# Kernel optimization log

Measured on AMD Instinct MI355X. Metric: run time of the kernel, lower is better.

## Reference

```python
import jax, jax.numpy as jnp
import numpy as np


def setup_inputs() -> dict:
    key = jax.random.key(0)
    k1, k2 = jax.random.split(key)
    B, S, D = 4, 2048, 1024
    x = jax.random.normal(k1, (B, S, D), dtype=jnp.float32)
    # uniform initializer in keras is small; scale to keep softmax well-behaved
    kernel = jax.random.normal(k2, (3, D, D), dtype=jnp.float32) * 0.02
    return {"x": x, "kernel": kernel}


def reference(x, kernel):
    # x: [B, S, D], kernel: [3, D, D]
    D = x.shape[-1]
    q = jnp.einsum('bsd,de->bse', x, kernel[0])
    k = jnp.einsum('bsd,de->bse', x, kernel[1])
    v = jnp.einsum('bsd,de->bse', x, kernel[2])
    scores = jnp.einsum('bqe,bke->bqk', q, k) / jnp.sqrt(jnp.float32(D))
    attn = jax.nn.softmax(scores, axis=-1)
    return jnp.einsum('bqk,bke->bqe', attn, v)
```

## Files before the change

kernel.cpp:

```cpp
#include <hip/hip_runtime.h>
#include <hip/hip_bf16.h>
#include <cstdint>

typedef __bf16 bf16x8 __attribute__((ext_vector_type(8)));
typedef float f32x4 __attribute__((ext_vector_type(4)));

__device__ __forceinline__ unsigned short f2bf(float f) {
  union { float f; uint32_t u; } a; a.f = f;
  uint32_t r = a.u + 0x7fffu + ((a.u >> 16) & 1u);
  return (unsigned short)(r >> 16);
}
__device__ __forceinline__ void gload_lds16(const unsigned short* g, unsigned short* l) {
  __builtin_amdgcn_global_load_lds(
      (const __attribute__((address_space(1))) void*)g,
      (__attribute__((address_space(3))) void*)l, 16, 0, 0);
}

__global__ void cast_all(const float* __restrict__ x, const float* __restrict__ W,
                         unsigned short* __restrict__ xb, unsigned short* __restrict__ Wt) {
  __shared__ float tileW[64][65];
  const int bx = blockIdx.x;
  const int t = threadIdx.x;
  if (bx < 4096) {
    size_t i = ((size_t)bx * 256 + t) * 8;
    float4 a = *(const float4*)(x + i);
    float4 b = *(const float4*)(x + i + 4);
    uint4 o;
    o.x = (uint32_t)f2bf(a.x) | ((uint32_t)f2bf(a.y) << 16);
    o.y = (uint32_t)f2bf(a.z) | ((uint32_t)f2bf(a.w) << 16);
    o.z = (uint32_t)f2bf(b.x) | ((uint32_t)f2bf(b.y) << 16);
    o.w = (uint32_t)f2bf(b.z) | ((uint32_t)f2bf(b.w) << 16);
    *(uint4*)(xb + i) = o;
  } else {
    const int b = bx - 4096;
    const int z = b >> 8;
    const int rest = b & 255;
    const int bxx = rest & 15, byy = rest >> 4;
    const float* Wz = W + (size_t)z * 1048576;
    unsigned short* Wtz = Wt + (size_t)z * 1048576;
    const int x0 = bxx * 64, y0 = byy * 64;
    {
      const int r = t >> 4;
      const int c = (t & 15) * 4;
#pragma unroll
      for (int p = 0; p < 64; p += 16) {
        float4 v = *(const float4*)(Wz + (size_t)(y0 + p + r) * 1024 + x0 + c);
        tileW[p + r][c + 0] = v.x;
        tileW[p + r][c + 1] = v.y;
        tileW[p + r][c + 2] = v.z;
        tileW[p + r][c + 3] = v.w;
      }
    }
    __syncthreads();
    {
      const int dc = (t & 7) * 8;
#pragma unroll
      for (int p = 0; p < 64; p += 32) {
        const int e = p + (t >> 3);
        uint4 o;
        o.x = (uint32_t)f2bf(tileW[dc + 0][e]) | ((uint32_t)f2bf(tileW[dc + 1][e]) << 16);
        o.y = (uint32_t)f2bf(tileW[dc + 2][e]) | ((uint32_t)f2bf(tileW[dc + 3][e]) << 16);
        o.z = (uint32_t)f2bf(tileW[dc + 4][e]) | ((uint32_t)f2bf(tileW[dc + 5][e]) << 16);
        o.w = (uint32_t)f2bf(tileW[dc + 6][e]) | ((uint32_t)f2bf(tileW[dc + 7][e]) << 16);
        *(uint4*)(Wtz + (size_t)(x0 + e) * 1024 + y0 + dc) = o;
      }
    }
  }
}

__global__ void reduce_aux(const float* __restrict__ partial, float* __restrict__ rowinv) {
  const int r = blockIdx.x * 256 + threadIdx.x;
  float s = 0.f;
#pragma unroll
  for (int j = 0; j < 32; ++j) s += partial[(size_t)j * 8192 + r];
  rowinv[r] = 1.f / s;
}

template <int MODE>
__global__ void __launch_bounds__(256)
gemm_bt(const unsigned short* __restrict__ Aall,
        const unsigned short* __restrict__ Btall,
        void* __restrict__ Call, unsigned short* __restrict__ VtPtr,
        float* __restrict__ aux,
        int K, int ldc, long sA, long sB, long sC) {
  __shared__ unsigned short As[2][4096];
  __shared__ unsigned short Bs[2][4096];
  const int t = threadIdx.x;
  const int lane = t & 63;
  const int quad = lane >> 4;
  const int l15 = lane & 15;
  const int wave = t >> 6;
  const int wm = (wave >> 1) * 64;
  const int wn = (wave & 1) * 64;
  const int z = blockIdx.z;

  const unsigned short* A = Aall + (size_t)z * sA + (size_t)blockIdx.x * 128 * K;
  const unsigned short* Bt = Btall + (size_t)z * sB + (size_t)blockIdx.y * 128 * K;

  const int srow = t >> 2;
  const int scol = (((t & 3) ^ ((srow >> 1) & 3)) * 8);
  const unsigned short* ga = A + (size_t)srow * K + scol;
  const unsigned short* gb = Bt + (size_t)srow * K + scol;
  const size_t rowskip = (size_t)64 * K;

  const int aOff = (wm + l15) * 32 + (quad ^ ((l15 >> 1) & 3)) * 8;
  const int bOff = (wn + l15) * 32 + (quad ^ ((l15 >> 1) & 3)) * 8;

  f32x4 acc[4][4];
#pragma unroll
  for (int i = 0; i < 4; i++)
#pragma unroll
    for (int j = 0; j < 4; j++) acc[i][j] = (f32x4){0.f, 0.f, 0.f, 0.f};

  gload_lds16(ga, &As[0][t * 8]);
  gload_lds16(ga + rowskip, &As[0][2048 + t * 8]);
  gload_lds16(gb, &Bs[0][t * 8]);
  gload_lds16(gb + rowskip, &Bs[0][2048 + t * 8]);

  int buf = 0;
  for (int k0 = 0; k0 < K; k0 += 32, buf ^= 1) {
    __syncthreads();
    if (k0 + 32 < K) {
      const int kn = k0 + 32;
      gload_lds16(ga + kn, &As[buf ^ 1][t * 8]);
      gload_lds16(ga + rowskip + kn, &As[buf ^ 1][2048 + t * 8]);
      gload_lds16(gb + kn, &Bs[buf ^ 1][t * 8]);
      gload_lds16(gb + rowskip + kn, &Bs[buf ^ 1][2048 + t * 8]);
    }
    const unsigned short* aB = &As[buf][aOff];
    const unsigned short* bB = &Bs[buf][bOff];
    bf16x8 a[4], b[4];
#pragma unroll
    for (int i = 0; i < 4; i++) a[i] = *(const bf16x8*)(aB + i * 512);
#pragma unroll
    for (int j = 0; j < 4; j++) b[j] = *(const bf16x8*)(bB + j * 512);
#pragma unroll
    for (int i = 0; i < 4; i++)
#pragma unroll
      for (int j = 0; j < 4; j++)
        acc[i][j] = __builtin_amdgcn_mfma_f32_16x16x32_bf16(a[i], b[j], acc[i][j], 0, 0, 0);
  }

  const int mbase = blockIdx.x * 128 + wm + quad * 4;
  const int nbase = blockIdx.y * 128 + wn + l15;

  if (MODE == 4) {
    if (z < 2) {
      unsigned short* C = (unsigned short*)Call + (size_t)z * sC;
#pragma unroll
      for (int mi = 0; mi < 4; mi++)
#pragma unroll
        for (int ni = 0; ni < 4; ni++) {
          const int m = mbase + mi * 16, n = nbase + ni * 16;
#pragma unroll
          for (int r = 0; r < 4; r++)
            C[(size_t)(m + r) * ldc + n] = f2bf(acc[mi][ni][r]);
        }
    } else {
      unsigned short* C = VtPtr;
#pragma unroll
      for (int mi = 0; mi < 4; mi++) {
        const int m = mbase + mi * 16;
        const int b = m >> 11, s = m & 2047;
#pragma unroll
        for (int ni = 0; ni < 4; ni++) {
          const int n = nbase + ni * 16;
          uint2 val;
          val.x = (uint32_t)f2bf(acc[mi][ni][0]) | ((uint32_t)f2bf(acc[mi][ni][1]) << 16);
          val.y = (uint32_t)f2bf(acc[mi][ni][2]) | ((uint32_t)f2bf(acc[mi][ni][3]) << 16);
          *(uint2*)(C + (size_t)b * 2097152 + (size_t)n * 2048 + s) = val;
        }
      }
    }
  } else {
    float* C = (float*)Call + (size_t)z * sC;
#pragma unroll
    for (int mi = 0; mi < 4; mi++) {
#pragma unroll
      for (int r = 0; r < 4; r++) {
        const int m = mbase + mi * 16 + r;
        const float inv = aux[(size_t)z * 2048 + m];
#pragma unroll
        for (int ni = 0; ni < 4; ni++)
          C[(size_t)m * ldc + nbase + ni * 16] = acc[mi][ni][r] * inv;
      }
    }
  }
}

__global__ void __launch_bounds__(512, 2)
gemm8_scores(const unsigned short* __restrict__ Aall,
             const unsigned short* __restrict__ Btall,
             unsigned short* __restrict__ Call, float* __restrict__ aux,
             int K, int ldc, long sA, long sB, long sC, float scale) {
  __shared__ unsigned short As[2][2][8192];
  __shared__ unsigned short Bs[2][2][8192];
  const int t = threadIdx.x;
  const int lane = t & 63;
  const int quad = lane >> 4;
  const int l15 = lane & 15;
  const int wave = t >> 6;
  const int wm = wave >> 2;
  const int wn = wave & 3;
  const int z = blockIdx.z;
  const int NT = K >> 6;

  const unsigned short* Ab = Aall + (size_t)z * sA + (size_t)blockIdx.x * 256 * K;
  const unsigned short* Bb = Btall + (size_t)z * sB + (size_t)blockIdx.y * 256 * K;

  const int sc = (((t & 3) ^ ((t >> 3) & 3)) * 8);
  const unsigned short* gA = Ab + (size_t)(t >> 2) * K + sc;
  const unsigned short* gB = Bb + (size_t)(t >> 2) * K + sc;
  const size_t half2 = (size_t)128 * K;

  const int swz = (quad ^ ((l15 >> 1) & 3)) * 8;
  const int aRd = (wm * 128 + l15) * 32 + swz;
  const int bRd = (wn * 64 + l15) * 32 + swz;

  f32x4 acc[8][4];
#pragma unroll
  for (int i = 0; i < 8; ++i)
#pragma unroll
    for (int j = 0; j < 4; ++j) acc[i][j] = (f32x4){0.f, 0.f, 0.f, 0.f};

#define STG_A(TT, KH) do { \
    const unsigned short* g_ = gA + (TT) * 64 + (KH) * 32; \
    unsigned short* d_ = &As[(TT) & 1][KH][t * 8]; \
    gload_lds16(g_, d_); \
    gload_lds16(g_ + half2, d_ + 4096); \
  } while (0)
#define STG_B(TT, KH) do { \
    const unsigned short* g_ = gB + (TT) * 64 + (KH) * 32; \
    unsigned short* d_ = &Bs[(TT) & 1][KH][t * 8]; \
    gload_lds16(g_, d_); \
    gload_lds16(g_ + half2, d_ + 4096); \
  } while (0)
#define PHASE_OPEN() do { \
    __builtin_amdgcn_sched_barrier(0); \
    __builtin_amdgcn_s_barrier(); \
    asm volatile("s_waitcnt lgkmcnt(0)" ::: "memory"); \
    __builtin_amdgcn_sched_barrier(0); \
    __builtin_amdgcn_s_setprio(1); \
  } while (0)
#define PHASE_CLOSE() do { \
    __builtin_amdgcn_s_setprio(0); \
    __builtin_amdgcn_sched_barrier(0); \
    __builtin_amdgcn_s_barrier(); \
  } while (0)

  STG_B(0, 0); STG_A(0, 0); STG_B(0, 1); STG_A(0, 1);
  STG_B(1, 0); STG_A(1, 0); STG_B(1, 1);
  asm volatile("s_waitcnt vmcnt(6)" ::: "memory");
  __builtin_amdgcn_s_barrier();

  for (int kt = 0; kt < NT; ++kt) {
    const int buf = kt & 1;
    bf16x8 bb[4], a[4];

#pragma unroll
    for (int j = 0; j < 4; ++j) bb[j] = *(const bf16x8*)&Bs[buf][0][bRd + j * 512];
#pragma unroll
    for (int i = 0; i < 4; ++i) a[i] = *(const bf16x8*)&As[buf][0][aRd + i * 512];
    if (kt + 1 < NT) STG_A(kt + 1, 1);
    PHASE_OPEN();
#pragma unroll
    for (int i = 0; i < 4; ++i)
#pragma unroll
      for (int j = 0; j < 4; ++j)
        acc[i][j] = __builtin_amdgcn_mfma_f32_16x16x32_bf16(a[i], bb[j], acc[i][j], 0, 0, 0);
    PHASE_CLOSE();

#pragma unroll
    for (int i = 0; i < 4; ++i) a[i] = *(const bf16x8*)&As[buf][0][aRd + 2048 + i * 512];
    if (kt + 2 < NT) STG_B(kt + 2, 0);
    PHASE_OPEN();
#pragma unroll
    for (int i = 0; i < 4; ++i)
#pragma unroll
      for (int j = 0; j < 4; ++j)
        acc[4 + i][j] = __builtin_amdgcn_mfma_f32_16x16x32_bf16(a[i], bb[j], acc[4 + i][j], 0, 0, 0);
    PHASE_CLOSE();

#pragma unroll
    for (int j = 0; j < 4; ++j) bb[j] = *(const bf16x8*)&Bs[buf][1][bRd + j * 512];
#pragma unroll
    for (int i = 0; i < 4; ++i) a[i] = *(const bf16x8*)&As[buf][1][aRd + i * 512];
    if (kt + 2 < NT) STG_A(kt + 2, 0);
    PHASE_OPEN();
#pragma unroll
    for (int i = 0; i < 4; ++i)
#pragma unroll
      for (int j = 0; j < 4; ++j)
        acc[i][j] = __builtin_amdgcn_mfma_f32_16x16x32_bf16(a[i], bb[j], acc[i][j], 0, 0, 0);
    PHASE_CLOSE();

#pragma unroll
    for (int i = 0; i < 4; ++i) a[i] = *(const bf16x8*)&As[buf][1][aRd + 2048 + i * 512];
    if (kt + 2 < NT) STG_B(kt + 2, 1);
    __builtin_amdgcn_sched_barrier(0);
    __builtin_amdgcn_s_barrier();
    asm volatile("s_waitcnt lgkmcnt(0)" ::: "memory");
    __builtin_amdgcn_sched_barrier(0);
    __builtin_amdgcn_s_setprio(1);
#pragma unroll
    for (int i = 0; i < 4; ++i)
#pragma unroll
      for (int j = 0; j < 4; ++j)
        acc[4 + i][j] = __builtin_amdgcn_mfma_f32_16x16x32_bf16(a[i], bb[j], acc[4 + i][j], 0, 0, 0);
    __builtin_amdgcn_s_setprio(0);
    __builtin_amdgcn_sched_barrier(0);
    if (kt < NT - 2) {
      asm volatile("s_waitcnt vmcnt(6)" ::: "memory");
    } else if (kt == NT - 2) {
      asm volatile("s_waitcnt vmcnt(0)" ::: "memory");
    }
    __builtin_amdgcn_s_barrier();
  }
#undef STG_A
#undef STG_B
#undef PHASE_OPEN
#undef PHASE_CLOSE

  const int mb = blockIdx.x * 256 + wm * 128 + quad * 4;
  const int nb = blockIdx.y * 256 + wn * 64 + l15;
  const int j = blockIdx.y * 4 + wn;
#pragma unroll
  for (int mi = 0; mi < 8; ++mi) {
#pragma unroll
    for (int r = 0; r < 4; ++r) {
      const int m = mb + mi * 16 + r;
      float s = 0.f;
#pragma unroll
      for (int ni = 0; ni < 4; ++ni) {
        const float e = __expf(acc[mi][ni][r] * scale);
        Call[(size_t)z * sC + (size_t)m * ldc + nb + ni * 16] = f2bf(e);
        s += e;
      }
      s += __shfl_xor(s, 1);
      s += __shfl_xor(s, 2);
      s += __shfl_xor(s, 4);
      s += __shfl_xor(s, 8);
      if (l15 == 0) aux[(size_t)j * 8192 + (size_t)z * 2048 + m] = s;
    }
  }
}

extern "C" void kernel_launch(void* const* d_in, const int* in_sizes, int n_in,
                              void* d_out, int out_size, void* d_ws, size_t ws_size,
                              hipStream_t stream) {
  const float* x = (const float*)d_in[0];
  const float* W = (const float*)d_in[1];
  float* out = (float*)d_out;
  char* ws = (char*)d_ws;
  unsigned short* xb = (unsigned short*)(ws);
  unsigned short* Wt = (unsigned short*)(ws + (16ll << 20));
  float* partial     = (float*)(ws + (16ll << 20));
  float* rowinv      = (float*)(ws + (18ll << 20));
  unsigned short* Q  = (unsigned short*)(ws + (22ll << 20));
  unsigned short* Kb = (unsigned short*)(ws + (38ll << 20));
  unsigned short* Vt = (unsigned short*)(ws + (54ll << 20));
  unsigned short* Sb = (unsigned short*)(ws + (70ll << 20));

  cast_all<<<4864, 256, 0, stream>>>(x, W, xb, Wt);

  gemm_bt<4><<<dim3(64, 8, 3), 256, 0, stream>>>(
      xb, Wt, Q, Vt, nullptr, 1024, 1024, 0L, 1048576L, 8388608L);
  gemm8_scores<<<dim3(8, 8, 4), 512, 0, stream>>>(
      Q, Kb, Sb, partial, 1024, 2048, 2097152L, 2097152L, 4194304L, 0.03125f);
  reduce_aux<<<32, 256, 0, stream>>>(partial, rowinv);
  gemm_bt<6><<<dim3(16, 8, 4), 256, 0, stream>>>(
      Sb, Vt, out, nullptr, rowinv, 2048, 1024, 4194304L, 2097152L, 2097152L);
}
```

Before: 241.9 us.

## Fuse x bf16 cast into QKV GEMM and add pipelined PV GEMM

Removes the standalone x-to-bf16 cast pass by loading fp32 x directly in the QKV projection GEMM, converting in registers and storing to LDS. The final attention-times-V GEMM is replaced by a 512-thread, 128x256-tile kernel with staged async global-to-LDS loads and priority-raised MFMA phases, reusing the scores kernel's phase macros. This trades the cast kernel's memory round trip for higher fp32 read traffic and register pressure in the QKV GEMM, and aims for better MFMA utilisation in the PV stage.

Measured after the change: 250.9 us. 3.7% more time.

```diff
diff --git a/kernel.cpp b/kernel.cpp
--- a/kernel.cpp
+++ b/kernel.cpp
@@ -10,60 +10,49 @@
   uint32_t r = a.u + 0x7fffu + ((a.u >> 16) & 1u);
   return (unsigned short)(r >> 16);
 }
+__device__ __forceinline__ uint32_t pk2(float lo, float hi) {
+  return (uint32_t)f2bf(lo) | ((uint32_t)f2bf(hi) << 16);
+}
 __device__ __forceinline__ void gload_lds16(const unsigned short* g, unsigned short* l) {
   __builtin_amdgcn_global_load_lds(
       (const __attribute__((address_space(1))) void*)g,
       (__attribute__((address_space(3))) void*)l, 16, 0, 0);
 }
 
-__global__ void cast_all(const float* __restrict__ x, const float* __restrict__ W,
-                         unsigned short* __restrict__ xb, unsigned short* __restrict__ Wt) {
+__global__ void cast_w(const float* __restrict__ W, unsigned short* __restrict__ Wt) {
   __shared__ float tileW[64][65];
-  const int bx = blockIdx.x;
+  const int b = blockIdx.x;
   const int t = threadIdx.x;
-  if (bx < 4096) {
-    size_t i = ((size_t)bx * 256 + t) * 8;
-    float4 a = *(const float4*)(x + i);
-    float4 b = *(const float4*)(x + i + 4);
-    uint4 o;
-    o.x = (uint32_t)f2bf(a.x) | ((uint32_t)f2bf(a.y) << 16);
-    o.y = (uint32_t)f2bf(a.z) | ((uint32_t)f2bf(a.w) << 16);
-    o.z = (uint32_t)f2bf(b.x) | ((uint32_t)f2bf(b.y) << 16);
-    o.w = (uint32_t)f2bf(b.z) | ((uint32_t)f2bf(b.w) << 16);
-    *(uint4*)(xb + i) = o;
-  } else {
-    const int b = bx - 4096;
-    const int z = b >> 8;
-    const int rest = b & 255;
-    const int bxx = rest & 15, byy = rest >> 4;
-    const float* Wz = W + (size_t)z * 1048576;
-    unsigned short* Wtz = Wt + (size_t)z * 1048576;
-    const int x0 = bxx * 64, y0 = byy * 64;
-    {
-      const int r = t >> 4;
-      const int c = (t & 15) * 4;
-#pragma unroll
-      for (int p = 0; p < 64; p += 16) {
-        float4 v = *(const float4*)(Wz + (size_t)(y0 + p + r) * 1024 + x0 + c);
-        tileW[p + r][c + 0] = v.x;
-        tileW[p + r][c + 1] = v.y;
-        tileW[p + r][c + 2] = v.z;
-        tileW[p + r][c + 3] = v.w;
-      }
-    }
-    __syncthreads();
-    {
-      const int dc = (t & 7) * 8;
-#pragma unroll
-      for (int p = 0; p < 64; p += 32) {
-        const int e = p + (t >> 3);
-        uint4 o;
-        o.x = (uint32_t)f2bf(tileW[dc + 0][e]) | ((uint32_t)f2bf(tileW[dc + 1][e]) << 16);
-        o.y = (uint32_t)f2bf(tileW[dc + 2][e]) | ((uint32_t)f2bf(tileW[dc + 3][e]) << 16);
-        o.z = (uint32_t)f2bf(tileW[dc + 4][e]) | ((uint32_t)f2bf(tileW[dc + 5][e]) << 16);
-        o.w = (uint32_t)f2bf(tileW[dc + 6][e]) | ((uint32_t)f2bf(tileW[dc + 7][e]) << 16);
-        *(uint4*)(Wtz + (size_t)(x0 + e) * 1024 + y0 + dc) = o;
-      }
+  const int z = b >> 8;
+  const int rest = b & 255;
+  const int bxx = rest & 15, byy = rest >> 4;
+  const float* Wz = W + (size_t)z * 1048576;
+  unsigned short* Wtz = Wt + (size_t)z * 1048576;
+  const int x0 = bxx * 64, y0 = byy * 64;
+  {
+    const int r = t >> 4;
+    const int c = (t & 15) * 4;
+#pragma unroll
+    for (int p = 0; p < 64; p += 16) {
+      float4 v = *(const float4*)(Wz + (size_t)(y0 + p + r) * 1024 + x0 + c);
+      tileW[p + r][c + 0] = v.x;
+      tileW[p + r][c + 1] = v.y;
+      tileW[p + r][c + 2] = v.z;
+      tileW[p + r][c + 3] = v.w;
+    }
+  }
+  __syncthreads();
+  {
+    const int dc = (t & 7) * 8;
+#pragma unroll
+    for (int p = 0; p < 64; p += 32) {
+      const int e = p + (t >> 3);
+      uint4 o;
+      o.x = pk2(tileW[dc + 0][e], tileW[dc + 1][e]);
+      o.y = pk2(tileW[dc + 2][e], tileW[dc + 3][e]);
+      o.z = pk2(tileW[dc + 4][e], tileW[dc + 5][e]);
+      o.w = pk2(tileW[dc + 6][e], tileW[dc + 7][e]);
+      *(uint4*)(Wtz + (size_t)(x0 + e) * 1024 + y0 + dc) = o;
     }
   }
 }
@@ -76,13 +65,9 @@
   rowinv[r] = 1.f / s;
 }
 
-template <int MODE>
 __global__ void __launch_bounds__(256)
-gemm_bt(const unsigned short* __restrict__ Aall,
-        const unsigned short* __restrict__ Btall,
-        void* __restrict__ Call, unsigned short* __restrict__ VtPtr,
-        float* __restrict__ aux,
-        int K, int ldc, long sA, long sB, long sC) {
+gemm_qkv(const float* __restrict__ X, const unsigned short* __restrict__ Wtall,
+         unsigned short* __restrict__ QK, unsigned short* __restrict__ Vt) {
   __shared__ unsigned short As[2][4096];
   __shared__ unsigned short Bs[2][4096];
   const int t = threadIdx.x;
@@ -94,14 +79,12 @@
   const int wn = (wave & 1) * 64;
   const int z = blockIdx.z;
 
-  const unsigned short* A = Aall + (size_t)z * sA + (size_t)blockIdx.x * 128 * K;
-  const unsigned short* Bt = Btall + (size_t)z * sB + (size_t)blockIdx.y * 128 * K;
+  const unsigned short* Bt = Wtall + (size_t)z * 1048576 + (size_t)blockIdx.y * 131072;
 
   const int srow = t >> 2;
   const int scol = (((t & 3) ^ ((srow >> 1) & 3)) * 8);
-  const unsigned short* ga = A + (size_t)srow * K + scol;
-  const unsigned short* gb = Bt + (size_t)srow * K + scol;
-  const size_t rowskip = (size_t)64 * K;
+  const float* gx = X + (size_t)(blockIdx.x * 128 + srow) * 1024 + scol;
+  const unsigned short* gb = Bt + (size_t)srow * 1024 + scol;
 
   const int aOff = (wm + l15) * 32 + (quad ^ ((l15 >> 1) & 3)) * 8;
   const int bOff = (wn + l15) * 32 + (quad ^ ((l15 >> 1) & 3)) * 8;
@@ -112,20 +95,33 @@
 #pragma unroll
     for (int j = 0; j < 4; j++) acc[i][j] = (f32x4){0.f, 0.f, 0.f, 0.f};
 
-  gload_lds16(ga, &As[0][t * 8]);
-  gload_lds16(ga + rowskip, &As[0][2048 + t * 8]);
+  float4 ar0, ar1, ar2, ar3;
+#define LOADA(KN) do {                                        \
+    ar0 = *(const float4*)(gx + (KN));                        \
+    ar1 = *(const float4*)(gx + (KN) + 4);                    \
+    ar2 = *(const float4*)(gx + 65536 + (KN));                \
+    ar3 = *(const float4*)(gx + 65536 + (KN) + 4);            \
+  } while (0)
+
+  LOADA(0);
   gload_lds16(gb, &Bs[0][t * 8]);
-  gload_lds16(gb + rowskip, &Bs[0][2048 + t * 8]);
+  gload_lds16(gb + 65536, &Bs[0][2048 + t * 8]);
 
   int buf = 0;
-  for (int k0 = 0; k0 < K; k0 += 32, buf ^= 1) {
+  for (int k0 = 0; k0 < 1024; k0 += 32, buf ^= 1) {
+    uint4 w0, w1;
+    w0.x = pk2(ar0.x, ar0.y); w0.y = pk2(ar0.z, ar0.w);
+    w0.z = pk2(ar1.x, ar1.y); w0.w = pk2(ar1.z, ar1.w);
+    w1.x = pk2(ar2.x, ar2.y); w1.y = pk2(ar2.z, ar2.w);
+    w1.z = pk2(ar3.x, ar3.y); w1.w = pk2(ar3.z, ar3.w);
+    *(uint4*)(&As[buf][t * 8]) = w0;
+    *(uint4*)(&As[buf][2048 + t * 8]) = w1;
     __syncthreads();
-    if (k0 + 32 < K) {
+    if (k0 + 32 < 1024) {
       const int kn = k0 + 32;
-      gload_lds16(ga + kn, &As[buf ^ 1][t * 8]);
-      gload_lds16(ga + rowskip + kn, &As[buf ^ 1][2048 + t * 8]);
+      LOADA(kn);
       gload_lds16(gb + kn, &Bs[buf ^ 1][t * 8]);
-      gload_lds16(gb + rowskip + kn, &Bs[buf ^ 1][2048 + t * 8]);
+      gload_lds16(gb + 65536 + kn, &Bs[buf ^ 1][2048 + t * 8]);
     }
     const unsigned short* aB = &As[buf][aOff];
     const unsigned short* bB = &Bs[buf][bOff];
@@ -140,49 +136,34 @@
       for (int j = 0; j < 4; j++)
         acc[i][j] = __builtin_amdgcn_mfma_f32_16x16x32_bf16(a[i], b[j], acc[i][j], 0, 0, 0);
   }
+#undef LOADA
 
   const int mbase = blockIdx.x * 128 + wm + quad * 4;
   const int nbase = blockIdx.y * 128 + wn + l15;
 
-  if (MODE == 4) {
-    if (z < 2) {
-      unsigned short* C = (unsigned short*)Call + (size_t)z * sC;
-#pragma unroll
-      for (int mi = 0; mi < 4; mi++)
-#pragma unroll
-        for (int ni = 0; ni < 4; ni++) {
-          const int m = mbase + mi * 16, n = nbase + ni * 16;
-#pragma unroll
-          for (int r = 0; r < 4; r++)
-            C[(size_t)(m + r) * ldc + n] = f2bf(acc[mi][ni][r]);
-        }
-    } else {
-      unsigned short* C = VtPtr;
-#pragma unroll
-      for (int mi = 0; mi < 4; mi++) {
-        const int m = mbase + mi * 16;
-        const int b = m >> 11, s = m & 2047;
-#pragma unroll
-        for (int ni = 0; ni < 4; ni++) {
-          const int n = nbase + ni * 16;
-          uint2 val;
-          val.x = (uint32_t)f2bf(acc[mi][ni][0]) | ((uint32_t)f2bf(acc[mi][ni][1]) << 16);
-          val.y = (uint32_t)f2bf(acc[mi][ni][2]) | ((uint32_t)f2bf(acc[mi][ni][3]) << 16);
-          *(uint2*)(C + (size_t)b * 2097152 + (size_t)n * 2048 + s) = val;
-        }
+  if (z < 2) {
+    unsigned short* C = QK + (size_t)z * 8388608;
+#pragma unroll
+    for (int mi = 0; mi < 4; mi++)
+#pragma unroll
+      for (int ni = 0; ni < 4; ni++) {
+        const int m = mbase + mi * 16, n = nbase + ni * 16;
+#pragma unroll
+        for (int r = 0; r < 4; r++)
+          C[(size_t)(m + r) * 1024 + n] = f2bf(acc[mi][ni][r]);
       }
-    }
   } else {
-    float* C = (float*)Call + (size_t)z * sC;
 #pragma unroll
     for (int mi = 0; mi < 4; mi++) {
-#pragma unroll
-      for (int r = 0; r < 4; r++) {
-        const int m = mbase + mi * 16 + r;
-        const float inv = aux[(size_t)z * 2048 + m];
-#pragma unroll
-        for (int ni = 0; ni < 4; ni++)
-          C[(size_t)m * ldc + nbase + ni * 16] = acc[mi][ni][r] * inv;
+      const int m = mbase + mi * 16;
+      const int b = m >> 11, s = m & 2047;
+#pragma unroll
+      for (int ni = 0; ni < 4; ni++) {
+        const int n = nbase + ni * 16;
+        uint2 val;
+        val.x = pk2(acc[mi][ni][0], acc[mi][ni][1]);
+        val.y = pk2(acc[mi][ni][2], acc[mi][ni][3]);
+        *(uint2*)(Vt + (size_t)b * 2097152 + (size_t)n * 2048 + s) = val;
       }
     }
   }
@@ -318,8 +299,6 @@
   }
 #undef STG_A
 #undef STG_B
-#undef PHASE_OPEN
-#undef PHASE_CLOSE
 
   const int mb = blockIdx.x * 256 + wm * 128 + quad * 4;
   const int nb = blockIdx.y * 256 + wn * 64 + l15;
@@ -345,6 +324,114 @@
   }
 }
 
+__global__ void __launch_bounds__(512, 2)
+gemm8_pv(const unsigned short* __restrict__ Aall,
+         const unsigned short* __restrict__ Btall,
+         float* __restrict__ Call, const float* __restrict__ rowinv) {
+  const int K = 2048, NT = 32;
+  __shared__ unsigned short As[2][2][4096];
+  __shared__ unsigned short Bs[2][2][8192];
+  const int t = threadIdx.x;
+  const int lane = t & 63;
+  const int quad = lane >> 4;
+  const int l15 = lane & 15;
+  const int wave = t >> 6;
+  const int wm = wave >> 2;
+  const int wn = wave & 3;
+  const int z = blockIdx.z;
+
+  const unsigned short* Ab = Aall + (size_t)z * 4194304 + (size_t)blockIdx.x * 128 * K;
+  const unsigned short* Bb = Btall + (size_t)z * 2097152 + (size_t)blockIdx.y * 256 * K;
+
+  const int sc = (((t & 3) ^ ((t >> 3) & 3)) * 8);
+  const unsigned short* gA = Ab + (size_t)(t >> 2) * K + sc;
+  const unsigned short* gB = Bb + (size_t)(t >> 2) * K + sc;
+  const size_t bhalf = (size_t)128 * K;
+
+  const int swz = (quad ^ ((l15 >> 1) & 3)) * 8;
+  const int aRd = (wm * 64 + l15) * 32 + swz;
+  const int bRd = (wn * 64 + l15) * 32 + swz;
+
+  f32x4 acc[4][4];
+#pragma unroll
+  for (int i = 0; i < 4; ++i)
+#pragma unroll
+    for (int j = 0; j < 4; ++j) acc[i][j] = (f32x4){0.f, 0.f, 0.f, 0.f};
+
+#define STGA(TT, KH) gload_lds16(gA + (TT) * 64 + (KH) * 32, &As[(TT) & 1][KH][t * 8])
+#define STGB(TT, KH) do { \
+    const unsigned short* g_ = gB + (TT) * 64 + (KH) * 32; \
+    unsigned short* d_ = &Bs[(TT) & 1][KH][t * 8]; \
+    gload_lds16(g_, d_); \
+    gload_lds16(g_ + bhalf, d_ + 4096); \
+  } while (0)
+
+  STGB(0, 0); STGA(0, 0); STGB(0, 1); STGA(0, 1);
+  STGB(1, 0); STGA(1, 0);
+  asm volatile("s_waitcnt vmcnt(3)" ::: "memory");
+  __builtin_amdgcn_s_barrier();
+
+  for (int kt = 0; kt < NT; ++kt) {
+    const int buf = kt & 1;
+    bf16x8 bb[4], a[4];
+
+#pragma unroll
+    for (int j = 0; j < 4; ++j) bb[j] = *(const bf16x8*)&Bs[buf][0][bRd + j * 512];
+#pragma unroll
+    for (int i = 0; i < 4; ++i) a[i] = *(const bf16x8*)&As[buf][0][aRd + i * 512];
+    if (kt + 1 < NT) { STGB(kt + 1, 1); STGA(kt + 1, 1); }
+    PHASE_OPEN();
+#pragma unroll
+    for (int i = 0; i < 4; ++i)
+#pragma unroll
+      for (int j = 0; j < 4; ++j)
+        acc[i][j] = __builtin_amdgcn_mfma_f32_16x16x32_bf16(a[i], bb[j], acc[i][j], 0, 0, 0);
+    PHASE_CLOSE();
+
+#pragma unroll
+    for (int j = 0; j < 4; ++j) bb[j] = *(const bf16x8*)&Bs[buf][1][bRd + j * 512];
+#pragma unroll
+    for (int i = 0; i < 4; ++i) a[i] = *(const bf16x8*)&As[buf][1][aRd + i * 512];
+    if (kt + 2 < NT) { STGB(kt + 2, 0); STGA(kt + 2, 0); }
+    __builtin_amdgcn_sched_barrier(0);
+    __builtin_amdgcn_s_barrier();
+    asm volatile("s_waitcnt lgkmcnt(0)" ::: "memory");
+    __builtin_amdgcn_sched_barrier(0);
+    __builtin_amdgcn_s_setprio(1);
+#pragma unroll
+    for (int i = 0; i < 4; ++i)
+#pragma unroll
+      for (int j = 0; j < 4; ++j)
+        acc[i][j] = __builtin_amdgcn_mfma_f32_16x16x32_bf16(a[i], bb[j], acc[i][j], 0, 0, 0);
+    __builtin_amdgcn_s_setprio(0);
+    __builtin_amdgcn_sched_barrier(0);
+    if (kt < NT - 2) {
+      asm volatile("s_waitcnt vmcnt(3)" ::: "memory");
+    } else if (kt == NT - 2) {
+      asm volatile("s_waitcnt vmcnt(0)" ::: "memory");
+    }
+    __builtin_amdgcn_s_barrier();
+  }
+#undef STGA
+#undef STGB
+#undef PHASE_OPEN
+#undef PHASE_CLOSE
+
+  const int mb = blockIdx.x * 128 + wm * 64 + quad * 4;
+  const int nb = blockIdx.y * 256 + wn * 64 + l15;
+#pragma unroll
+  for (int mi = 0; mi < 4; ++mi) {
+#pragma unroll
+    for (int r = 0; r < 4; ++r) {
+      const int m = mb + mi * 16 + r;
+      const float inv = rowinv[(size_t)z * 2048 + m];
+#pragma unroll
+      for (int ni = 0; ni < 4; ++ni)
+        Call[(size_t)z * 2097152 + (size_t)m * 1024 + nb + ni * 16] = acc[mi][ni][r] * inv;
+    }
+  }
+}
+
 extern "C" void kernel_launch(void* const* d_in, const int* in_sizes, int n_in,
                               void* d_out, int out_size, void* d_ws, size_t ws_size,
                               hipStream_t stream) {
@@ -352,7 +439,6 @@
   const float* W = (const float*)d_in[1];
   float* out = (float*)d_out;
   char* ws = (char*)d_ws;
-  unsigned short* xb = (unsigned short*)(ws);
   unsigned short* Wt = (unsigned short*)(ws + (16ll << 20));
   float* partial     = (float*)(ws + (16ll << 20));
   float* rowinv      = (float*)(ws + (18ll << 20));
@@ -360,14 +446,16 @@
   unsigned short* Kb = (unsigned short*)(ws + (38ll << 20));
   unsigned short* Vt = (unsigned short*)(ws + (54ll << 20));
   unsigned short* Sb = (unsigned short*)(ws + (70ll << 20));
-
-  cast_all<<<4864, 256, 0, stream>>>(x, W, xb, Wt);
-
-  gemm_bt<4><<<dim3(64, 8, 3), 256, 0, stream>>>(
-      xb, Wt, Q, Vt, nullptr, 1024, 1024, 0L, 1048576L, 8388608L);
+  (void)Kb;
+
+  cast_w<<<768, 256, 0, stream>>>(W, Wt);
+
+  gemm_qkv<<<dim3(64, 8, 3), 256, 0, stream>>>(x, Wt, Q, Vt);
+
   gemm8_scores<<<dim3(8, 8, 4), 512, 0, stream>>>(
-      Q, Kb, Sb, partial, 1024, 2048, 2097152L, 2097152L, 4194304L, 0.03125f);
+      Q, Q + 8388608, Sb, partial, 1024, 2048, 2097152L, 2097152L, 4194304L, 0.03125f);
+
   reduce_aux<<<32, 256, 0, stream>>>(partial, rowinv);
-  gemm_bt<6><<<dim3(16, 8, 4), 256, 0, stream>>>(
-      Sb, Vt, out, nullptr, rowinv, 2048, 1024, 4194304L, 2097152L, 2097152L);
-}
+
+  gemm8_pv<<<dim3(16, 4, 4), 512, 0, stream>>>(Sb, Vt, out, rowinv);
+}
```
